# Optimization experiments

Hardware: AMD Instinct MI355X
Metric: run time of the kernel (lower is better)

Reference implementation:

```python
import jax, jax.numpy as jnp
import numpy as np
from jax import lax

BN_EPS = 1e-5

def conv_bn_prelu(x, w, b, scale, bias, a):
    # Conv2d(k=3, pad=1, stride=1) in NCHW / OIHW layout
    y = lax.conv_general_dilated(x, w, window_strides=(1, 1), padding='SAME',
                                 dimension_numbers=('NCHW', 'OIHW', 'NCHW'))
    y = y + b[None, :, None, None]
    # BatchNorm2d, training-mode batch statistics over (B, H, W)
    mean = jnp.mean(y, axis=(0, 2, 3), keepdims=True)
    var = jnp.var(y, axis=(0, 2, 3), keepdims=True)
    y = (y - mean) * lax.rsqrt(var + BN_EPS)
    y = y * scale[None, :, None, None] + bias[None, :, None, None]
    # PReLU with single shared slope parameter
    return jnp.where(y >= 0, y, a * y)

def setup_inputs() -> dict:
    key = jax.random.key(0)
    ks = jax.random.split(key, 7)
    B, C, H, W = 4, 64, 64, 64
    x = jax.random.normal(ks[0], (B, C, H, W), dtype=jnp.float32)
    conv_w = jax.random.normal(ks[1], (C, C, 3, 3), dtype=jnp.float32) * 0.05
    conv_b = jax.random.normal(ks[2], (C,), dtype=jnp.float32) * 0.05
    bn_scale = jax.random.uniform(ks[3], (C,), dtype=jnp.float32, minval=0.5, maxval=1.5)
    bn_bias = jax.random.normal(ks[4], (C,), dtype=jnp.float32) * 0.05
    prelu_a = jnp.full((1,), 0.25, dtype=jnp.float32)
    gamma = jax.random.normal(ks[5], (1,), dtype=jnp.float32)
    return {'x': x, 'conv_w': conv_w, 'conv_b': conv_b, 'bn_scale': bn_scale,
            'bn_bias': bn_bias, 'prelu_a': prelu_a, 'gamma': gamma}

def reference(x, conv_w, conv_b, bn_scale, bn_bias, prelu_a, gamma):
    B, C, H, W = x.shape
    N = H * W
    feat = conv_bn_prelu(x, conv_w, conv_b, bn_scale, bn_bias, prelu_a)  # (B,C,H,W)
    f = feat.reshape(B, C, N)  # proj_query = f^T, proj_key = f, proj_value = f
    # energy[b,i,j] = sum_c f[b,c,i] * f[b,c,j]  -> (B, N, N)
    energy = jnp.einsum('bci,bcj->bij', f, f)
    # energy_new = rowmax - energy, softmax over last dim
    energy_new = jnp.max(energy, axis=-1, keepdims=True) - energy
    attn = jax.nn.softmax(energy_new, axis=-1)
    # out = bmm(proj_value, attention^T): out[b,c,i] = sum_j f[b,c,j] * attn[b,i,j]
    out = jnp.einsum('bcj,bij->bci', f, attn).reshape(B, C, H, W)
    return gamma * out + feat
```

## Files before the change

### kernel.cpp

```cpp
#include <hip/hip_runtime.h>

constexpr int kB = 4, kC = 64, kH = 64, kW = 64, kN = kH * kW;
constexpr float kEps = 1e-5f;
constexpr int SPLIT = 4;
constexpr float kQS = 1.2011224087864498f;

#if __has_builtin(__builtin_amdgcn_exp2f)
#define EXP2F(x) __builtin_amdgcn_exp2f(x)
#else
#define EXP2F(x) exp2f(x)
#endif

typedef __attribute__((ext_vector_type(8))) short short8;
typedef __attribute__((ext_vector_type(4))) float f32x4;
typedef unsigned short u16;

__device__ inline unsigned pkbf(float a, float b) {
  unsigned ua = __float_as_uint(a), ub = __float_as_uint(b);
  ua += 0x7fff + ((ua >> 16) & 1);
  ub += 0x7fff + ((ub >> 16) & 1);
  return (ua >> 16) | (ub & 0xffff0000u);
}

__global__ __launch_bounds__(256) void prep_w_kernel(const float* __restrict__ w,
                                                     u16* __restrict__ wA,
                                                     float* __restrict__ stat) {
  if (blockIdx.x == 0) {
    stat[threadIdx.x] = 0.f;
    stat[256 + threadIdx.x] = 0.f;
  }
  int idx = blockIdx.x * 256 + threadIdx.x;
  if (idx < 64 * 576) {
    int oc = idx / 576, r = idx - oc * 576;
    int khw = r >> 6, ic = r & 63;
    float v = w[(oc * 64 + ic) * 9 + khw];
    unsigned u = __float_as_uint(v);
    u += 0x7fff + ((u >> 16) & 1);
    wA[idx] = (u16)(u >> 16);
  }
}

__global__ __launch_bounds__(256) void conv_kernel(const float* __restrict__ x,
                                                   const u16* __restrict__ wA,
                                                   const float* __restrict__ bias,
                                                   float* __restrict__ y,
                                                   float* __restrict__ stat) {
  const int tid = threadIdx.x;
  const int lane = tid & 63;
  const int wv = tid >> 6;
  const int bx = blockIdx.x;
  const int b = bx >> 7;
  const int h = (bx & 127) >> 1;
  const int w0 = (bx & 1) * 32;
  const int lw = lane & 15, lg = lane >> 4;

  __shared__ __align__(16) u16 xt[3 * 40 * 64];

#pragma unroll
  for (int rep = 0; rep < 4; ++rep) {
    int idx = rep * 256 + tid;
    if (idx < 960) {
      int kh = idx / 320;
      int t = idx - kh * 320;
      int gw = t >> 5, icp = t & 31;
      int wb = w0 - 4 + gw * 4;
      int hh = h + kh - 1;
      float4 va = {0.f, 0.f, 0.f, 0.f}, vb = {0.f, 0.f, 0.f, 0.f};
      if (hh >= 0 && hh < 64 && wb >= 0 && wb < 64) {
        va = *(const float4*)&x[((b * 64 + icp * 2) * 64 + hh) * 64 + wb];
        vb = *(const float4*)&x[((b * 64 + icp * 2 + 1) * 64 + hh) * 64 + wb];
      }
      float av[4] = {va.x, va.y, va.z, va.w};
      float bv[4] = {vb.x, vb.y, vb.z, vb.w};
#pragma unroll
      for (int j = 0; j < 4; ++j) {
        int wc = gw * 4 + j;
        *(unsigned*)&xt[(kh * 40 + wc) * 64 + (((icp >> 2) ^ (wc & 7)) * 8 + (icp & 3) * 2)] =
            pkbf(av[j], bv[j]);
      }
    }
  }
  __syncthreads();

  const int oc0 = wv * 16;
  short8 af[18];
#pragma unroll
  for (int kc = 0; kc < 18; ++kc)
    af[kc] = *(const short8*)&wA[(oc0 + lw) * 576 + kc * 32 + lg * 8];

  f32x4 acc[2];
  acc[0] = (f32x4){0.f, 0.f, 0.f, 0.f};
  acc[1] = (f32x4){0.f, 0.f, 0.f, 0.f};
#pragma unroll
  for (int kc = 0; kc < 18; ++kc) {
    const int khw = kc >> 1;
    const int kh = khw / 3, kwv = khw % 3;
#pragma unroll
    for (int nt = 0; nt < 2; ++nt) {
      int wc = nt * 16 + lw + kwv + 3;
      short8 bf = *(const short8*)&xt[(kh * 40 + wc) * 64 + ((((kc & 1) * 4 + lg) ^ (wc & 7)) * 8)];
      acc[nt] = __builtin_amdgcn_mfma_f32_16x16x32_bf16(af[kc], bf, acc[nt], 0, 0, 0);
    }
  }

  float* st = stat + (bx & 3) * 128;
#pragma unroll
  for (int r = 0; r < 4; ++r) {
    const int oc = oc0 + lg * 4 + r;
    const float bz = bias[oc];
    float v0 = acc[0][r] + bz;
    float v1 = acc[1][r] + bz;
    y[((b * 64 + oc) * 64 + h) * 64 + w0 + lw] = v0;
    y[((b * 64 + oc) * 64 + h) * 64 + w0 + 16 + lw] = v1;
    float s = v0 + v1, q = v0 * v0 + v1 * v1;
#pragma unroll
    for (int m = 1; m < 16; m <<= 1) {
      s += __shfl_xor(s, m);
      q += __shfl_xor(q, m);
    }
    if (lw == 0) {
      atomicAdd(&st[oc], s);
      atomicAdd(&st[64 + oc], q);
    }
  }
}

__global__ __launch_bounds__(256) void pack_kernel(const float* __restrict__ y,
                                                   const float* __restrict__ stat,
                                                   const float* __restrict__ scale,
                                                   const float* __restrict__ bias,
                                                   const float* __restrict__ pa,
                                                   float* __restrict__ ABg,
                                                   u16* __restrict__ fbfA,
                                                   u16* __restrict__ fbfB) {
  __shared__ float ls[64 * 65];
  __shared__ float sAB[128];
  const int tid = threadIdx.x;
  const int b = blockIdx.x >> 6;
  const int n0 = (blockIdx.x & 63) << 6;
  if (tid < 64) {
    const float inv_n = 1.f / (float)(kB * kN);
    float ssum = stat[tid] + stat[128 + tid] + stat[256 + tid] + stat[384 + tid];
    float qsum = stat[64 + tid] + stat[192 + tid] + stat[320 + tid] + stat[448 + tid];
    float mean = ssum * inv_n;
    float var = qsum * inv_n - mean * mean;
    float A = scale[tid] * rsqrtf(var + kEps);
    float Bc = bias[tid] - mean * A;
    sAB[tid] = A;
    sAB[64 + tid] = Bc;
    ABg[tid] = A;
    ABg[64 + tid] = Bc;
  }
  __syncthreads();
  {
    const int c = tid >> 2, nj = (tid & 3) << 4;
    const float A = sAB[c], Bc = sAB[64 + c], a = pa[0];
    const float* yp = y + ((b * kC + c) * kN) + n0 + nj;
    float f[16];
#pragma unroll
    for (int v = 0; v < 4; ++v) {
      float4 xv = *(const float4*)(yp + v * 4);
      float t;
      t = fmaf(A, xv.x, Bc); f[v * 4 + 0] = t >= 0.f ? t : a * t;
      t = fmaf(A, xv.y, Bc); f[v * 4 + 1] = t >= 0.f ? t : a * t;
      t = fmaf(A, xv.z, Bc); f[v * 4 + 2] = t >= 0.f ? t : a * t;
      t = fmaf(A, xv.w, Bc); f[v * 4 + 3] = t >= 0.f ? t : a * t;
    }
#pragma unroll
    for (int v = 0; v < 16; ++v) ls[c * 65 + nj + v] = f[v];
  }
  __syncthreads();
  {
    int chunk = tid >> 5, pt = chunk >> 1, kc = chunk & 1;
    int lp2 = (tid & 31) * 2;
    u16* dst = fbfA + ((size_t)((b * 256 + (n0 >> 4) + pt) * 2 + kc)) * 512;
#pragma unroll
    for (int e = 0; e < 2; ++e) {
      int L = lp2 + e;
      int n = pt * 16 + (L & 15);
      int cb = kc * 32 + (L >> 4) * 8;
      float v[8];
#pragma unroll
      for (int r = 0; r < 8; ++r) v[r] = kQS * ls[(cb + r) * 65 + n];
      uint4 o = {pkbf(v[0], v[1]), pkbf(v[2], v[3]), pkbf(v[4], v[5]), pkbf(v[6], v[7])};
      *(uint4*)&dst[L * 8] = o;
    }
  }
  {
    int chunk = tid >> 5, jt = chunk >> 2, ct = chunk & 3;
    int lp2 = (tid & 31) * 2;
    u16* dst = fbfB + ((size_t)((b * 128 + (n0 >> 5) + jt) * 4 + ct)) * 512;
#pragma unroll
    for (int e = 0; e < 2; ++e) {
      int L = lp2 + e;
      int c = ct * 16 + (L & 15);
      int nb = jt * 32 + (L >> 4) * 8;
      float v[8];
#pragma unroll
      for (int r = 0; r < 8; ++r) v[r] = ls[c * 65 + nb + r];
      uint4 o = {pkbf(v[0], v[1]), pkbf(v[2], v[3]), pkbf(v[4], v[5]), pkbf(v[6], v[7])};
      *(uint4*)&dst[L * 8] = o;
    }
  }
}

__global__ __launch_bounds__(256, 2) void attn_kernel(const u16* __restrict__ fbfA,
                                                      const u16* __restrict__ fbfB,
                                                      float* __restrict__ Op,
                                                      float* __restrict__ lp) {
  const int tid = threadIdx.x;
  const int lane = tid & 63;
  const int w = tid >> 6;
  const int bx = blockIdx.x;
  const int s = bx & 3, itb = (bx >> 2) & 15, b = bx >> 6;
  const int c15 = lane & 15, g = lane >> 4;

  __shared__ __align__(16) u16 Ps[4][64 * 40];
  u16* ps = &Ps[w][0];
  const int pw_off = c15 * 40 + g * 4;
  const int pr_off = c15 * 40 + g * 8;

  const uint4* fA = (const uint4*)fbfA;
  const uint4* fB = (const uint4*)fbfB;

  uint4 qf[4][2];
  const int ptq = itb * 16 + w * 4;
#pragma unroll
  for (int it = 0; it < 4; ++it)
#pragma unroll
    for (int kc = 0; kc < 2; ++kc) {
      uint4 q = fA[(size_t)((b * 256 + ptq + it) * 2 + kc) * 64 + lane];
      q.x ^= 0x80008000u; q.y ^= 0x80008000u; q.z ^= 0x80008000u; q.w ^= 0x80008000u;
      qf[it][kc] = q;
    }

  const short8 ones = {0x3F80, 0x3F80, 0x3F80, 0x3F80, 0x3F80, 0x3F80, 0x3F80, 0x3F80};

  f32x4 oacc[4][4];
  f32x4 lacc[4];
#pragma unroll
  for (int it = 0; it < 4; ++it) {
    lacc[it] = (f32x4){0.f, 0.f, 0.f, 0.f};
#pragma unroll
    for (int ct = 0; ct < 4; ++ct) oacc[it][ct] = (f32x4){0.f, 0.f, 0.f, 0.f};
  }

#pragma unroll 2
  for (int jj = 0; jj < 32; ++jj) {
    const int j0 = (s * 32 + jj) * 32;
    const int ca = (b * 256 + (j0 >> 4)) * 2;
    uint4 a00 = fA[(size_t)(ca + 0) * 64 + lane];
    uint4 a01 = fA[(size_t)(ca + 1) * 64 + lane];
    uint4 a10 = fA[(size_t)(ca + 2) * 64 + lane];
    uint4 a11 = fA[(size_t)(ca + 3) * 64 + lane];
    const int cb = (b * 128 + (j0 >> 5)) * 4;
    uint4 v0 = fB[(size_t)(cb + 0) * 64 + lane];
    uint4 v1 = fB[(size_t)(cb + 1) * 64 + lane];
    uint4 v2 = fB[(size_t)(cb + 2) * 64 + lane];
    uint4 v3 = fB[(size_t)(cb + 3) * 64 + lane];

    f32x4 sv[2][4];
#pragma unroll
    for (int it = 0; it < 4; ++it) {
      f32x4 z0 = (f32x4){0.f, 0.f, 0.f, 0.f};
      z0 = __builtin_amdgcn_mfma_f32_16x16x32_bf16(*(short8*)&a00, *(short8*)&qf[it][0], z0, 0, 0, 0);
      z0 = __builtin_amdgcn_mfma_f32_16x16x32_bf16(*(short8*)&a01, *(short8*)&qf[it][1], z0, 0, 0, 0);
      sv[0][it] = z0;
      f32x4 z1 = (f32x4){0.f, 0.f, 0.f, 0.f};
      z1 = __builtin_amdgcn_mfma_f32_16x16x32_bf16(*(short8*)&a10, *(short8*)&qf[it][0], z1, 0, 0, 0);
      z1 = __builtin_amdgcn_mfma_f32_16x16x32_bf16(*(short8*)&a11, *(short8*)&qf[it][1], z1, 0, 0, 0);
      sv[1][it] = z1;
    }
#pragma unroll
    for (int it = 0; it < 4; ++it)
#pragma unroll
      for (int jt = 0; jt < 2; ++jt) {
        float p0 = EXP2F(sv[jt][it][0]);
        float p1 = EXP2F(sv[jt][it][1]);
        float p2 = EXP2F(sv[jt][it][2]);
        float p3 = EXP2F(sv[jt][it][3]);
        uint2 d;
        d.x = __builtin_amdgcn_perm(__float_as_uint(p1), __float_as_uint(p0), 0x07060302u);
        d.y = __builtin_amdgcn_perm(__float_as_uint(p3), __float_as_uint(p2), 0x07060302u);
        *(uint2*)&ps[pw_off + it * 640 + jt * 16] = d;
      }
#pragma unroll
    for (int it = 0; it < 4; ++it) {
      short8 pf = *(const short8*)&ps[pr_off + it * 640];
      lacc[it] = __builtin_amdgcn_mfma_f32_16x16x32_bf16(pf, ones, lacc[it], 0, 0, 0);
      oacc[it][0] = __builtin_amdgcn_mfma_f32_16x16x32_bf16(pf, *(short8*)&v0, oacc[it][0], 0, 0, 0);
      oacc[it][1] = __builtin_amdgcn_mfma_f32_16x16x32_bf16(pf, *(short8*)&v1, oacc[it][1], 0, 0, 0);
      oacc[it][2] = __builtin_amdgcn_mfma_f32_16x16x32_bf16(pf, *(short8*)&v2, oacc[it][2], 0, 0, 0);
      oacc[it][3] = __builtin_amdgcn_mfma_f32_16x16x32_bf16(pf, *(short8*)&v3, oacc[it][3], 0, 0, 0);
    }
  }

  const int rbase = (s * kB + b) * kN + itb * 256 + w * 64;
  float* Ow = Op + (size_t)rbase * 64;
#pragma unroll
  for (int it = 0; it < 4; ++it)
#pragma unroll
    for (int ct = 0; ct < 4; ++ct)
#pragma unroll
      for (int r = 0; r < 4; ++r)
        Ow[(it * 16 + g * 4 + r) * 64 + ct * 16 + c15] = oacc[it][ct][r];
  if (c15 == 0) {
    float* lw_ = lp + rbase;
#pragma unroll
    for (int it = 0; it < 4; ++it)
#pragma unroll
      for (int r = 0; r < 4; ++r) lw_[it * 16 + g * 4 + r] = lacc[it][r];
  }
}

__global__ __launch_bounds__(256) void combine_kernel(const float* __restrict__ Op,
                                                      const float* __restrict__ lp,
                                                      const float* __restrict__ y,
                                                      const float* __restrict__ ABg,
                                                      const float* __restrict__ pa,
                                                      const float* __restrict__ gamma_p,
                                                      float* __restrict__ out) {
  const int tid = threadIdx.x;
  const int bx = blockIdx.x;
  const int b = bx >> 6, it64 = bx & 63;
  const int i0 = it64 * 64;
  __shared__ float tr[64 * 65];
  __shared__ float linv[64];
  if (tid < 64) {
    float sum = 0.f;
    for (int s = 0; s < SPLIT; ++s) sum += lp[(size_t)(s * kB + b) * kN + i0 + tid];
    linv[tid] = 1.f / sum;
  }
  __syncthreads();
  const float gm = gamma_p[0];
  const float a = pa[0];
#pragma unroll
  for (int rr = 0; rr < 4; ++rr) {
    int flat4 = rr * 256 + tid;
    int i = flat4 >> 4, c4 = (flat4 & 15) * 4;
    float4 acc = {0.f, 0.f, 0.f, 0.f};
    for (int s = 0; s < SPLIT; ++s) {
      float4 v = *(const float4*)&Op[((size_t)(s * kB + b) * kN + i0 + i) * 64 + c4];
      acc.x += v.x; acc.y += v.y; acc.z += v.z; acc.w += v.w;
    }
    float sc = gm * linv[i];
    tr[(c4 + 0) * 65 + i] = acc.x * sc;
    tr[(c4 + 1) * 65 + i] = acc.y * sc;
    tr[(c4 + 2) * 65 + i] = acc.z * sc;
    tr[(c4 + 3) * 65 + i] = acc.w * sc;
  }
  __syncthreads();
#pragma unroll
  for (int rr = 0; rr < 4; ++rr) {
    int flat4 = rr * 256 + tid;
    int c = flat4 >> 4, i4 = (flat4 & 15) * 4;
    const float A = ABg[c], Bc = ABg[64 + c];
    float4 yv = *(const float4*)&y[(size_t)(b * 64 + c) * 4096 + it64 * 64 + i4];
    float t;
    float4 ov;
    t = fmaf(A, yv.x, Bc); t = t >= 0.f ? t : a * t; ov.x = tr[c * 65 + i4 + 0] + t;
    t = fmaf(A, yv.y, Bc); t = t >= 0.f ? t : a * t; ov.y = tr[c * 65 + i4 + 1] + t;
    t = fmaf(A, yv.z, Bc); t = t >= 0.f ? t : a * t; ov.z = tr[c * 65 + i4 + 2] + t;
    t = fmaf(A, yv.w, Bc); t = t >= 0.f ? t : a * t; ov.w = tr[c * 65 + i4 + 3] + t;
    *(float4*)&out[(size_t)(b * 64 + c) * 4096 + it64 * 64 + i4] = ov;
  }
}

extern "C" void kernel_launch(void* const* d_in, const int* in_sizes, int n_in,
                              void* d_out, int out_size, void* d_ws, size_t ws_size,
                              hipStream_t stream) {
  (void)in_sizes; (void)n_in; (void)out_size; (void)ws_size;
  const float* x        = (const float*)d_in[0];
  const float* conv_w   = (const float*)d_in[1];
  const float* conv_b   = (const float*)d_in[2];
  const float* bn_scale = (const float*)d_in[3];
  const float* bn_bias  = (const float*)d_in[4];
  const float* prelu_a  = (const float*)d_in[5];
  const float* gamma    = (const float*)d_in[6];
  float* out = (float*)d_out;

  u16* fbfA = (u16*)d_ws;
  u16* fbfB = fbfA + kB * kC * kN;
  float* stat = (float*)(fbfB + kB * kC * kN);
  float* ABg = stat + 512;
  u16* wA = (u16*)(ABg + 128);
  float* Op = (float*)(wA + 36864);
  float* lp = Op + (size_t)SPLIT * kB * kN * 64;

  float* y = out;

  prep_w_kernel<<<144, 256, 0, stream>>>(conv_w, wA, stat);
  conv_kernel<<<kB * kH * 2, 256, 0, stream>>>(x, wA, conv_b, y, stat);
  pack_kernel<<<kB * (kN / 64), 256, 0, stream>>>(y, stat, bn_scale, bn_bias, prelu_a,
                                                  ABg, fbfA, fbfB);
  attn_kernel<<<kB * 16 * SPLIT, 256, 0, stream>>>(fbfA, fbfB, Op, lp);
  combine_kernel<<<kB * 64, 256, 0, stream>>>(Op, lp, y, ABg, prelu_a, gamma, out);
}
```

Before: 126.1 us.

## Fuse split-K combine into attention kernel via per-tile atomic counter barrier

Removes the separate combine kernel launch. Each attention block, once its partial output is written, increments a per-(batch, row-tile) counter and spins until all SPLIT partner blocks are done. It then combines and writes one 64-row slice of the final output, reusing the Ps shared buffer as transpose scratch. This saves a launch and its gap but relies on all 256 blocks being co-resident to avoid deadlock, and adds spin-wait overhead.

```diff
diff --git a/kernel.cpp b/kernel.cpp
--- a/kernel.cpp
+++ b/kernel.cpp
@@ -24,10 +24,12 @@
 
 __global__ __launch_bounds__(256) void prep_w_kernel(const float* __restrict__ w,
                                                      u16* __restrict__ wA,
-                                                     float* __restrict__ stat) {
+                                                     float* __restrict__ stat,
+                                                     int* __restrict__ cnt) {
   if (blockIdx.x == 0) {
     stat[threadIdx.x] = 0.f;
     stat[256 + threadIdx.x] = 0.f;
+    if (threadIdx.x < 64) cnt[threadIdx.x] = 0;
   }
   int idx = blockIdx.x * 256 + threadIdx.x;
   if (idx < 64 * 576) {
@@ -207,7 +209,13 @@
 __global__ __launch_bounds__(256, 2) void attn_kernel(const u16* __restrict__ fbfA,
                                                       const u16* __restrict__ fbfB,
                                                       float* __restrict__ Op,
-                                                      float* __restrict__ lp) {
+                                                      float* __restrict__ lp,
+                                                      const float* __restrict__ y,
+                                                      const float* __restrict__ ABg,
+                                                      const float* __restrict__ pa,
+                                                      const float* __restrict__ gamma_p,
+                                                      int* __restrict__ cnt,
+                                                      float* __restrict__ out) {
   const int tid = threadIdx.x;
   const int lane = tid & 63;
   const int w = tid >> 6;
@@ -311,24 +319,25 @@
 #pragma unroll
       for (int r = 0; r < 4; ++r) lw_[it * 16 + g * 4 + r] = lacc[it][r];
   }
-}
-
-__global__ __launch_bounds__(256) void combine_kernel(const float* __restrict__ Op,
-                                                      const float* __restrict__ lp,
-                                                      const float* __restrict__ y,
-                                                      const float* __restrict__ ABg,
-                                                      const float* __restrict__ pa,
-                                                      const float* __restrict__ gamma_p,
-                                                      float* __restrict__ out) {
-  const int tid = threadIdx.x;
-  const int bx = blockIdx.x;
-  const int b = bx >> 6, it64 = bx & 63;
+
+  __threadfence();
+  __syncthreads();
+  int* cp = &cnt[b * 16 + itb];
+  if (tid == 0) {
+    atomicAdd(cp, 1);
+    while (__hip_atomic_load(cp, __ATOMIC_RELAXED, __HIP_MEMORY_SCOPE_AGENT) < SPLIT)
+      __builtin_amdgcn_s_sleep(2);
+  }
+  __syncthreads();
+  (void)__hip_atomic_load(cp, __ATOMIC_ACQUIRE, __HIP_MEMORY_SCOPE_AGENT);
+
+  float* tr = (float*)&Ps[0][0];
+  __shared__ float linv[64];
+  const int it64 = itb * 4 + s;
   const int i0 = it64 * 64;
-  __shared__ float tr[64 * 65];
-  __shared__ float linv[64];
   if (tid < 64) {
     float sum = 0.f;
-    for (int s = 0; s < SPLIT; ++s) sum += lp[(size_t)(s * kB + b) * kN + i0 + tid];
+    for (int ss = 0; ss < SPLIT; ++ss) sum += lp[(size_t)(ss * kB + b) * kN + i0 + tid];
     linv[tid] = 1.f / sum;
   }
   __syncthreads();
@@ -339,8 +348,8 @@
     int flat4 = rr * 256 + tid;
     int i = flat4 >> 4, c4 = (flat4 & 15) * 4;
     float4 acc = {0.f, 0.f, 0.f, 0.f};
-    for (int s = 0; s < SPLIT; ++s) {
-      float4 v = *(const float4*)&Op[((size_t)(s * kB + b) * kN + i0 + i) * 64 + c4];
+    for (int ss = 0; ss < SPLIT; ++ss) {
+      float4 v = *(const float4*)&Op[((size_t)(ss * kB + b) * kN + i0 + i) * 64 + c4];
       acc.x += v.x; acc.y += v.y; acc.z += v.z; acc.w += v.w;
     }
     float sc = gm * linv[i];
@@ -383,16 +392,17 @@
   u16* fbfB = fbfA + kB * kC * kN;
   float* stat = (float*)(fbfB + kB * kC * kN);
   float* ABg = stat + 512;
-  u16* wA = (u16*)(ABg + 128);
+  int* cnt = (int*)(ABg + 128);
+  u16* wA = (u16*)(cnt + 64);
   float* Op = (float*)(wA + 36864);
   float* lp = Op + (size_t)SPLIT * kB * kN * 64;
 
   float* y = out;
 
-  prep_w_kernel<<<144, 256, 0, stream>>>(conv_w, wA, stat);
+  prep_w_kernel<<<144, 256, 0, stream>>>(conv_w, wA, stat, cnt);
   conv_kernel<<<kB * kH * 2, 256, 0, stream>>>(x, wA, conv_b, y, stat);
   pack_kernel<<<kB * (kN / 64), 256, 0, stream>>>(y, stat, bn_scale, bn_bias, prelu_a,
                                                   ABg, fbfA, fbfB);
-  attn_kernel<<<kB * 16 * SPLIT, 256, 0, stream>>>(fbfA, fbfB, Op, lp);
-  combine_kernel<<<kB * 64, 256, 0, stream>>>(Op, lp, y, ABg, prelu_a, gamma, out);
-}
+  attn_kernel<<<kB * 16 * SPLIT, 256, 0, stream>>>(fbfA, fbfB, Op, lp, y, ABg,
+                                                   prelu_a, gamma, cnt, out);
+}
```

New measurement: 168.0 us. +33.2%, slower.

## Split attention key loop across two wave groups with LDS reduction

Applied to the files above, without the earlier changes.

Doubles the attention block to 512 threads. Two groups of four waves each take alternating key tiles for the same query rows, and their partial output and row-sum accumulators are combined through shared memory before the write. This targets low occupancy and parallelism in the attention kernel, which launches only 256 blocks, by putting more waves in flight per block. In exchange it adds two barriers, an 80KB shared-memory reduction buffer, and allows one block per CU.

```diff
diff --git a/kernel.cpp b/kernel.cpp
--- a/kernel.cpp
+++ b/kernel.cpp
@@ -204,19 +204,20 @@
   }
 }
 
-__global__ __launch_bounds__(256, 2) void attn_kernel(const u16* __restrict__ fbfA,
+__global__ __launch_bounds__(512, 1) void attn_kernel(const u16* __restrict__ fbfA,
                                                       const u16* __restrict__ fbfB,
                                                       float* __restrict__ Op,
                                                       float* __restrict__ lp) {
   const int tid = threadIdx.x;
   const int lane = tid & 63;
   const int w = tid >> 6;
+  const int wq = w & 3, jh = w >> 2;
   const int bx = blockIdx.x;
   const int s = bx & 3, itb = (bx >> 2) & 15, b = bx >> 6;
   const int c15 = lane & 15, g = lane >> 4;
 
-  __shared__ __align__(16) u16 Ps[4][64 * 40];
-  u16* ps = &Ps[w][0];
+  __shared__ __align__(16) float RedU[20480];
+  u16* ps = (u16*)RedU + w * 2560;
   const int pw_off = c15 * 40 + g * 4;
   const int pr_off = c15 * 40 + g * 8;
 
@@ -224,7 +225,7 @@
   const uint4* fB = (const uint4*)fbfB;
 
   uint4 qf[4][2];
-  const int ptq = itb * 16 + w * 4;
+  const int ptq = itb * 16 + wq * 4;
 #pragma unroll
   for (int it = 0; it < 4; ++it)
 #pragma unroll
@@ -246,7 +247,8 @@
   }
 
 #pragma unroll 2
-  for (int jj = 0; jj < 32; ++jj) {
+  for (int jj2 = 0; jj2 < 16; ++jj2) {
+    const int jj = jj2 * 2 + jh;
     const int j0 = (s * 32 + jj) * 32;
     const int ca = (b * 256 + (j0 >> 4)) * 2;
     uint4 a00 = fA[(size_t)(ca + 0) * 64 + lane];
@@ -295,21 +297,45 @@
     }
   }
 
-  const int rbase = (s * kB + b) * kN + itb * 256 + w * 64;
-  float* Ow = Op + (size_t)rbase * 64;
-#pragma unroll
-  for (int it = 0; it < 4; ++it)
-#pragma unroll
-    for (int ct = 0; ct < 4; ++ct)
-#pragma unroll
-      for (int r = 0; r < 4; ++r)
-        Ow[(it * 16 + g * 4 + r) * 64 + ct * 16 + c15] = oacc[it][ct][r];
-  if (c15 == 0) {
-    float* lw_ = lp + rbase;
+  __syncthreads();
+  if (jh == 1) {
+    float* dst = RedU + wq * 5120;
 #pragma unroll
     for (int it = 0; it < 4; ++it)
 #pragma unroll
-      for (int r = 0; r < 4; ++r) lw_[it * 16 + g * 4 + r] = lacc[it][r];
+      for (int ct = 0; ct < 4; ++ct)
+        *(f32x4*)&dst[(it * 4 + ct) * 256 + lane * 4] = oacc[it][ct];
+#pragma unroll
+    for (int it = 0; it < 4; ++it)
+      *(f32x4*)&dst[(16 + it) * 256 + lane * 4] = lacc[it];
+  }
+  __syncthreads();
+  if (jh == 0) {
+    const float* src = RedU + wq * 5120;
+#pragma unroll
+    for (int it = 0; it < 4; ++it) {
+#pragma unroll
+      for (int ct = 0; ct < 4; ++ct)
+        oacc[it][ct] = oacc[it][ct] + *(const f32x4*)&src[(it * 4 + ct) * 256 + lane * 4];
+      lacc[it] = lacc[it] + *(const f32x4*)&src[(16 + it) * 256 + lane * 4];
+    }
+
+    const int rbase = (s * kB + b) * kN + itb * 256 + wq * 64;
+    float* Ow = Op + (size_t)rbase * 64;
+#pragma unroll
+    for (int it = 0; it < 4; ++it)
+#pragma unroll
+      for (int ct = 0; ct < 4; ++ct)
+#pragma unroll
+        for (int r = 0; r < 4; ++r)
+          Ow[(it * 16 + g * 4 + r) * 64 + ct * 16 + c15] = oacc[it][ct][r];
+    if (c15 == 0) {
+      float* lw_ = lp + rbase;
+#pragma unroll
+      for (int it = 0; it < 4; ++it)
+#pragma unroll
+        for (int r = 0; r < 4; ++r) lw_[it * 16 + g * 4 + r] = lacc[it][r];
+    }
   }
 }
 
@@ -393,6 +419,6 @@
   conv_kernel<<<kB * kH * 2, 256, 0, stream>>>(x, wA, conv_b, y, stat);
   pack_kernel<<<kB * (kN / 64), 256, 0, stream>>>(y, stat, bn_scale, bn_bias, prelu_a,
                                                   ABg, fbfA, fbfB);
-  attn_kernel<<<kB * 16 * SPLIT, 256, 0, stream>>>(fbfA, fbfB, Op, lp);
+  attn_kernel<<<kB * 16 * SPLIT, 512, 0, stream>>>(fbfA, fbfB, Op, lp);
   combine_kernel<<<kB * 64, 256, 0, stream>>>(Op, lp, y, ABg, prelu_a, gamma, out);
 }
```

After: 123.9 us. No clear change (-1.7%).
